# Performance work log

Hardware: AMD Instinct MI355X
Metric: run time of the kernel (lower is better)

The kernel has to match this reference:

```python
import jax, jax.numpy as jnp
import numpy as np

B, D, H, T, F = 2, 256, 8, 128, 64
C = H * F          # channels = 512
TE = 512           # time_embed_dim


def setup_inputs() -> dict:
    key = jax.random.key(0)
    ks = jax.random.split(key, 9)
    pd = jax.random.randint(ks[2], (B, T, T), 0, 2 * T - 1, dtype=jnp.int32) - (T - 1)
    s = 0.02
    return {
        "qk": jax.random.normal(ks[0], (B, D, H, T, F), jnp.float32),
        "temb": jax.random.normal(ks[1], (B, T, TE), jnp.float32),
        "pairwise_distances": pd,
        "w_dist": jax.random.normal(ks[3], (3, C), jnp.float32) * s,
        "b_dist": jax.random.normal(ks[4], (C,), jnp.float32) * s,
        "w_time": jax.random.normal(ks[5], (TE, C), jnp.float32) * s,
        "b_time": jax.random.normal(ks[6], (C,), jnp.float32) * s,
        "w_out": jax.random.normal(ks[7], (C, C), jnp.float32) * s,
        "b_out": jax.random.normal(ks[8], (C,), jnp.float32) * s,
    }


def _rpe_net(temb, pd, w_dist, b_dist, w_time, b_time, w_out, b_out):
    d = pd.astype(jnp.float32)
    # (B, T, S, 3): log(1+d+), log(1+d-), indicator(d==0)
    dist_embs = jnp.stack(
        [jnp.log1p(jnp.maximum(d, 0.0)),
         jnp.log1p(jnp.maximum(-d, 0.0)),
         (pd == 0).astype(jnp.float32)],
        axis=-1,
    )
    emb = (temb @ w_time + b_time)[:, :, None, :] + dist_embs @ w_dist + b_dist  # (B,T,S,C)
    R = jax.nn.silu(emb) @ w_out + b_out  # (B,T,S,C)
    return R.reshape(*pd.shape, H, F)     # (B,T,S,H,F)


def reference(qk, temb, pairwise_distances, w_dist, b_dist, w_time, b_time, w_out, b_out):
    R = _rpe_net(temb, pairwise_distances, w_dist, b_dist, w_time, b_time, w_out, b_out)
    # forward_qk: contract head_dim f for every (t, s) pair
    return jnp.einsum('bdhtf,btshf->bdhts', qk, R)
```

## Files before the change

### kernel.cpp

```cpp
#include <hip/hip_runtime.h>
#include <hip/hip_bf16.h>

#define B_  2
#define D_  256
#define H_  8
#define T_  128
#define S_  128
#define F_  64
#define C_  512
#define TE_ 512

typedef _Float16 f16x8 __attribute__((ext_vector_type(8)));
typedef _Float16 f16x4 __attribute__((ext_vector_type(4)));
typedef float    f32x4 __attribute__((ext_vector_type(4)));

__global__ __launch_bounds__(256) void k_time_proj(
    const float* __restrict__ temb, const float* __restrict__ w_time,
    const float* __restrict__ b_time, const float* __restrict__ b_dist,
    float* __restrict__ tp)
{
    int row0 = blockIdx.x * 2;
    int tid  = threadIdx.x;
    __shared__ float te[2][TE_];
    for (int i = tid; i < 2 * TE_; i += 256)
        te[i >> 9][i & 511] = temb[(size_t)row0 * TE_ + i];
    __syncthreads();
    for (int half = 0; half < 2; ++half) {
        int c = tid + half * 256;
        float bias = b_time[c] + b_dist[c];
        float a0 = bias, a1 = bias;
        for (int e = 0; e < TE_; ++e) {
            float w = w_time[(size_t)e * C_ + c];
            a0 += te[0][e] * w;
            a1 += te[1][e] * w;
        }
        tp[(size_t)row0 * C_ + c]       = a0;
        tp[(size_t)(row0 + 1) * C_ + c] = a1;
    }
}

__global__ __launch_bounds__(256) void k_wt(
    const float* __restrict__ w_out, _Float16* __restrict__ Wt)
{
    __shared__ float tile[64][65];
    int bn = blockIdx.x;
    int bk = blockIdx.y;
    int tx = threadIdx.x & 63;
    int ty = threadIdx.x >> 6;
#pragma unroll
    for (int p = 0; p < 16; ++p) {
        int row = p * 4 + ty;
        tile[row][tx] = w_out[(size_t)(bk * 64 + row) * C_ + bn * 64 + tx];
    }
    __syncthreads();
#pragma unroll
    for (int p = 0; p < 16; ++p) {
        int row = p * 4 + ty;
        Wt[(size_t)(bn * 64 + row) * C_ + bk * 64 + tx] = (_Float16)tile[tx][row];
    }
}

__global__ __launch_bounds__(256) void k_rpe_gemm(
    const float* __restrict__ tp, const int* __restrict__ pd,
    const float* __restrict__ w_dist, const _Float16* __restrict__ Wt,
    const float* __restrict__ b_out, _Float16* __restrict__ R)
{
    __shared__ _Float16 As[128][72];
    __shared__ _Float16 Bs[128][72];
    __shared__ float fs[3][128];
    __shared__ float tps[C_];
    __shared__ float wds[3][C_];
    int bm = blockIdx.x, bn = blockIdx.y;
    int tid = threadIdx.x;

    if (tid < 128) {
        int d = pd[bm * 128 + tid];
        fs[0][tid] = log1pf(fmaxf((float)d, 0.f));
        fs[1][tid] = log1pf(fmaxf((float)(-d), 0.f));
        fs[2][tid] = (d == 0) ? 1.f : 0.f;
    }
    for (int i = tid; i < C_; i += 256) tps[i] = tp[(size_t)bm * C_ + i];
    for (int i = tid; i < 3 * C_; i += 256) wds[i >> 9][i & 511] = w_dist[i];
    __syncthreads();

    int wave = tid >> 6, lane = tid & 63;
    int wm = (wave >> 1) * 64, wn = (wave & 1) * 64;
    int mrow = lane & 15, kq = (lane >> 4) * 8;
    int srow  = tid >> 1;
    int khalf = (tid & 1) * 32;
    int lrow = tid >> 3, lcol = (tid & 7) * 8;
    float f0 = fs[0][srow], f1 = fs[1][srow], f2 = fs[2][srow];

    f32x4 acc[4][4] = {};
    for (int k0 = 0; k0 < C_; k0 += 64) {
        _Float16 abuf[32];
#pragma unroll
        for (int kk = 0; kk < 32; ++kk) {
            int k = k0 + khalf + kk;
            float e = tps[k] + f0 * wds[0][k] + f1 * wds[1][k] + f2 * wds[2][k];
            e = e / (1.f + __expf(-e));
            abuf[kk] = (_Float16)e;
        }
#pragma unroll
        for (int v = 0; v < 4; ++v)
            *(f16x8*)&As[srow][khalf + v * 8] = *(const f16x8*)&abuf[v * 8];
#pragma unroll
        for (int p = 0; p < 4; ++p) {
            int r = p * 32 + lrow;
            *(f16x8*)&Bs[r][lcol] = *(const f16x8*)&Wt[(size_t)(bn * 128 + r) * C_ + k0 + lcol];
        }
        __syncthreads();
#pragma unroll
        for (int ks = 0; ks < 64; ks += 32) {
            f16x8 af[4], bfr[4];
#pragma unroll
            for (int i = 0; i < 4; ++i) af[i]  = *(const f16x8*)&As[wm + i * 16 + mrow][ks + kq];
#pragma unroll
            for (int j = 0; j < 4; ++j) bfr[j] = *(const f16x8*)&Bs[wn + j * 16 + mrow][ks + kq];
#pragma unroll
            for (int i = 0; i < 4; ++i)
#pragma unroll
                for (int j = 0; j < 4; ++j)
                    acc[i][j] = __builtin_amdgcn_mfma_f32_16x16x32_f16(af[i], bfr[j], acc[i][j], 0, 0, 0);
        }
        __syncthreads();
    }
    int col = lane & 15, rb = (lane >> 4) * 4;
    const size_t arow0 = (size_t)bm * 128;
#pragma unroll
    for (int j = 0; j < 4; ++j) {
        int n = bn * 128 + wn + j * 16 + col;
        float bo = b_out[n];
#pragma unroll
        for (int i = 0; i < 4; ++i)
#pragma unroll
            for (int r = 0; r < 4; ++r) {
                size_t m = arow0 + wm + i * 16 + rb + r;
                R[m * C_ + n] = (_Float16)(acc[i][j][r] + bo);
            }
    }
}

__global__ __launch_bounds__(256) void k_einsum(
    const float* __restrict__ qk, const _Float16* __restrict__ R,
    float* __restrict__ out)
{
    int bht  = blockIdx.x;
    int dblk = blockIdx.y;
    int t = bht & 127;
    int h = (bht >> 7) & 7;
    int b = bht >> 10;
    int tid = threadIdx.x;
    int wave = tid >> 6, lane = tid & 63;
    int wm = (wave >> 1) * 64, wn = (wave & 1) * 64;
    int mrow = lane & 15, kq = (lane >> 4) * 8;

    const size_t HTF = (size_t)H_ * T_ * F_;
    const float* qbase = qk + (size_t)b * D_ * HTF + (size_t)h * (T_ * F_)
                       + (size_t)t * F_ + (size_t)(dblk * 128) * HTF;
    const _Float16* rbase = R + ((size_t)(b * T_ + t) * S_) * C_ + h * 64;

    f32x4 acc[4][4] = {};
#pragma unroll
    for (int ks = 0; ks < 64; ks += 32) {
        f16x8 af[4], bfr[4];
#pragma unroll
        for (int i = 0; i < 4; ++i) {
            const float* p = qbase + (size_t)(wm + i * 16 + mrow) * HTF + ks + kq;
            float4 v0 = *(const float4*)p;
            float4 v1 = *(const float4*)(p + 4);
            f16x8 a;
            a[0] = (_Float16)v0.x; a[1] = (_Float16)v0.y;
            a[2] = (_Float16)v0.z; a[3] = (_Float16)v0.w;
            a[4] = (_Float16)v1.x; a[5] = (_Float16)v1.y;
            a[6] = (_Float16)v1.z; a[7] = (_Float16)v1.w;
            af[i] = a;
        }
#pragma unroll
        for (int j = 0; j < 4; ++j)
            bfr[j] = *(const f16x8*)(rbase + (size_t)(wn + j * 16 + mrow) * C_ + ks + kq);
#pragma unroll
        for (int i = 0; i < 4; ++i)
#pragma unroll
            for (int j = 0; j < 4; ++j)
                acc[i][j] = __builtin_amdgcn_mfma_f32_16x16x32_f16(af[i], bfr[j], acc[i][j], 0, 0, 0);
    }

    const size_t obase = (size_t)b * ((size_t)D_ * H_ * T_ * S_) + (size_t)h * (T_ * S_)
                       + (size_t)t * S_ + (size_t)(dblk * 128) * ((size_t)H_ * T_ * S_);
    int col = lane & 15, rb = (lane >> 4) * 4;
#pragma unroll
    for (int i = 0; i < 4; ++i)
#pragma unroll
        for (int r = 0; r < 4; ++r) {
            int dloc = wm + i * 16 + rb + r;
            size_t o = obase + (size_t)dloc * ((size_t)H_ * T_ * S_);
#pragma unroll
            for (int j = 0; j < 4; ++j)
                out[o + wn + j * 16 + col] = acc[i][j][r];
        }
}

extern "C" void kernel_launch(void* const* d_in, const int* in_sizes, int n_in,
                              void* d_out, int out_size, void* d_ws, size_t ws_size,
                              hipStream_t stream) {
    (void)in_sizes; (void)n_in; (void)out_size; (void)ws_size;
    const float* qk     = (const float*)d_in[0];
    const float* temb   = (const float*)d_in[1];
    const int*   pd     = (const int*)d_in[2];
    const float* w_dist = (const float*)d_in[3];
    const float* b_dist = (const float*)d_in[4];
    const float* w_time = (const float*)d_in[5];
    const float* b_time = (const float*)d_in[6];
    const float* w_out  = (const float*)d_in[7];
    const float* b_out  = (const float*)d_in[8];
    float* out = (float*)d_out;

    char* ws = (char*)d_ws;
    float*     tp = (float*)ws;
    _Float16*  Wt = (_Float16*)(ws + 512 * 1024);
    _Float16*  R  = (_Float16*)(ws + 1024 * 1024);

    k_time_proj<<<dim3(B_ * T_ / 2), dim3(256), 0, stream>>>(temb, w_time, b_time, b_dist, tp);
    k_wt<<<dim3(8, 8), dim3(256), 0, stream>>>(w_out, Wt);
    k_rpe_gemm<<<dim3(256, 4), dim3(256), 0, stream>>>(tp, pd, w_dist, Wt, b_out, R);
    k_einsum<<<dim3(B_ * H_ * T_, 2), dim3(256), 0, stream>>>(qk, R, out);
}
```

Baseline: 541.8 us.

## Split embed+SiLU out of RPE GEMM, widen time projection, use nontemporal einsum IO

The SiLU embedding is no longer recomputed inside each GEMM tile for every N-block. It is now produced once by a separate kernel into a half-precision A buffer in workspace, which the GEMM then loads. The time-projection kernel now handles four rows per block, so each w_time load is reused more. The einsum kernel uses nontemporal loads for qk and nontemporal stores for the output to avoid polluting the cache. In exchange, an extra 32 MB buffer round-trips through memory, and there is one more kernel launch.

```diff
diff --git a/kernel.cpp b/kernel.cpp
--- a/kernel.cpp
+++ b/kernel.cpp
@@ -19,23 +19,33 @@
     const float* __restrict__ b_time, const float* __restrict__ b_dist,
     float* __restrict__ tp)
 {
-    int row0 = blockIdx.x * 2;
+    int row0 = blockIdx.x * 4;
     int tid  = threadIdx.x;
-    __shared__ float te[2][TE_];
-    for (int i = tid; i < 2 * TE_; i += 256)
+    __shared__ float te[4][TE_];
+    for (int i = tid; i < 4 * TE_; i += 256)
         te[i >> 9][i & 511] = temb[(size_t)row0 * TE_ + i];
     __syncthreads();
-    for (int half = 0; half < 2; ++half) {
-        int c = tid + half * 256;
-        float bias = b_time[c] + b_dist[c];
-        float a0 = bias, a1 = bias;
-        for (int e = 0; e < TE_; ++e) {
-            float w = w_time[(size_t)e * C_ + c];
-            a0 += te[0][e] * w;
-            a1 += te[1][e] * w;
-        }
-        tp[(size_t)row0 * C_ + c]       = a0;
-        tp[(size_t)(row0 + 1) * C_ + c] = a1;
+    int c0 = tid, c1 = tid + 256;
+    float bias0 = b_time[c0] + b_dist[c0];
+    float bias1 = b_time[c1] + b_dist[c1];
+    float a[4][2];
+#pragma unroll
+    for (int r = 0; r < 4; ++r) { a[r][0] = bias0; a[r][1] = bias1; }
+#pragma unroll 4
+    for (int e = 0; e < TE_; ++e) {
+        float w0 = w_time[(size_t)e * C_ + c0];
+        float w1 = w_time[(size_t)e * C_ + c1];
+#pragma unroll
+        for (int r = 0; r < 4; ++r) {
+            float t = te[r][e];
+            a[r][0] += t * w0;
+            a[r][1] += t * w1;
+        }
+    }
+#pragma unroll
+    for (int r = 0; r < 4; ++r) {
+        tp[(size_t)(row0 + r) * C_ + c0] = a[r][0];
+        tp[(size_t)(row0 + r) * C_ + c1] = a[r][1];
     }
 }
 
@@ -60,54 +70,59 @@
     }
 }
 
-__global__ __launch_bounds__(256) void k_rpe_gemm(
+__global__ __launch_bounds__(256) void k_embed_silu(
     const float* __restrict__ tp, const int* __restrict__ pd,
-    const float* __restrict__ w_dist, const _Float16* __restrict__ Wt,
+    const float* __restrict__ w_dist, _Float16* __restrict__ A)
+{
+    int row = blockIdx.x * 8 + (threadIdx.x >> 5);
+    int bt  = row >> 7;
+    int d   = pd[row];
+    float f0 = log1pf(fmaxf((float)d, 0.f));
+    float f1 = log1pf(fmaxf((float)(-d), 0.f));
+    float f2 = (d == 0) ? 1.f : 0.f;
+    int c0 = (threadIdx.x & 31) * 16;
+    _Float16 buf[16];
+#pragma unroll
+    for (int v = 0; v < 4; ++v) {
+        int c = c0 + v * 4;
+        float4 t4 = *(const float4*)&tp[(size_t)bt * C_ + c];
+        float4 w0 = *(const float4*)&w_dist[c];
+        float4 w1 = *(const float4*)&w_dist[C_ + c];
+        float4 w2 = *(const float4*)&w_dist[2 * C_ + c];
+        float e0 = t4.x + f0 * w0.x + f1 * w1.x + f2 * w2.x;
+        float e1 = t4.y + f0 * w0.y + f1 * w1.y + f2 * w2.y;
+        float e2 = t4.z + f0 * w0.z + f1 * w1.z + f2 * w2.z;
+        float e3 = t4.w + f0 * w0.w + f1 * w1.w + f2 * w2.w;
+        buf[v * 4 + 0] = (_Float16)(e0 / (1.f + __expf(-e0)));
+        buf[v * 4 + 1] = (_Float16)(e1 / (1.f + __expf(-e1)));
+        buf[v * 4 + 2] = (_Float16)(e2 / (1.f + __expf(-e2)));
+        buf[v * 4 + 3] = (_Float16)(e3 / (1.f + __expf(-e3)));
+    }
+    *(f16x8*)&A[(size_t)row * C_ + c0]     = *(const f16x8*)&buf[0];
+    *(f16x8*)&A[(size_t)row * C_ + c0 + 8] = *(const f16x8*)&buf[8];
+}
+
+__global__ __launch_bounds__(256) void k_gemm_R(
+    const _Float16* __restrict__ A, const _Float16* __restrict__ Wt,
     const float* __restrict__ b_out, _Float16* __restrict__ R)
 {
+    const int K = 512, N = 512;
     __shared__ _Float16 As[128][72];
     __shared__ _Float16 Bs[128][72];
-    __shared__ float fs[3][128];
-    __shared__ float tps[C_];
-    __shared__ float wds[3][C_];
     int bm = blockIdx.x, bn = blockIdx.y;
     int tid = threadIdx.x;
-
-    if (tid < 128) {
-        int d = pd[bm * 128 + tid];
-        fs[0][tid] = log1pf(fmaxf((float)d, 0.f));
-        fs[1][tid] = log1pf(fmaxf((float)(-d), 0.f));
-        fs[2][tid] = (d == 0) ? 1.f : 0.f;
-    }
-    for (int i = tid; i < C_; i += 256) tps[i] = tp[(size_t)bm * C_ + i];
-    for (int i = tid; i < 3 * C_; i += 256) wds[i >> 9][i & 511] = w_dist[i];
-    __syncthreads();
-
     int wave = tid >> 6, lane = tid & 63;
     int wm = (wave >> 1) * 64, wn = (wave & 1) * 64;
     int mrow = lane & 15, kq = (lane >> 4) * 8;
-    int srow  = tid >> 1;
-    int khalf = (tid & 1) * 32;
     int lrow = tid >> 3, lcol = (tid & 7) * 8;
-    float f0 = fs[0][srow], f1 = fs[1][srow], f2 = fs[2][srow];
-
+    const size_t arow0 = (size_t)bm * 128;
     f32x4 acc[4][4] = {};
-    for (int k0 = 0; k0 < C_; k0 += 64) {
-        _Float16 abuf[32];
-#pragma unroll
-        for (int kk = 0; kk < 32; ++kk) {
-            int k = k0 + khalf + kk;
-            float e = tps[k] + f0 * wds[0][k] + f1 * wds[1][k] + f2 * wds[2][k];
-            e = e / (1.f + __expf(-e));
-            abuf[kk] = (_Float16)e;
-        }
-#pragma unroll
-        for (int v = 0; v < 4; ++v)
-            *(f16x8*)&As[srow][khalf + v * 8] = *(const f16x8*)&abuf[v * 8];
+    for (int k0 = 0; k0 < K; k0 += 64) {
 #pragma unroll
         for (int p = 0; p < 4; ++p) {
             int r = p * 32 + lrow;
-            *(f16x8*)&Bs[r][lcol] = *(const f16x8*)&Wt[(size_t)(bn * 128 + r) * C_ + k0 + lcol];
+            *(f16x8*)&As[r][lcol] = *(const f16x8*)&A[(arow0 + r) * K + k0 + lcol];
+            *(f16x8*)&Bs[r][lcol] = *(const f16x8*)&Wt[(size_t)(bn * 128 + r) * K + k0 + lcol];
         }
         __syncthreads();
 #pragma unroll
@@ -126,7 +141,6 @@
         __syncthreads();
     }
     int col = lane & 15, rb = (lane >> 4) * 4;
-    const size_t arow0 = (size_t)bm * 128;
 #pragma unroll
     for (int j = 0; j < 4; ++j) {
         int n = bn * 128 + wn + j * 16 + col;
@@ -136,7 +150,7 @@
 #pragma unroll
             for (int r = 0; r < 4; ++r) {
                 size_t m = arow0 + wm + i * 16 + rb + r;
-                R[m * C_ + n] = (_Float16)(acc[i][j][r] + bo);
+                R[m * N + n] = (_Float16)(acc[i][j][r] + bo);
             }
     }
 }
@@ -166,14 +180,14 @@
         f16x8 af[4], bfr[4];
 #pragma unroll
         for (int i = 0; i < 4; ++i) {
-            const float* p = qbase + (size_t)(wm + i * 16 + mrow) * HTF + ks + kq;
-            float4 v0 = *(const float4*)p;
-            float4 v1 = *(const float4*)(p + 4);
+            const f32x4* p = (const f32x4*)(qbase + (size_t)(wm + i * 16 + mrow) * HTF + ks + kq);
+            f32x4 v0 = __builtin_nontemporal_load(p);
+            f32x4 v1 = __builtin_nontemporal_load(p + 1);
             f16x8 a;
-            a[0] = (_Float16)v0.x; a[1] = (_Float16)v0.y;
-            a[2] = (_Float16)v0.z; a[3] = (_Float16)v0.w;
-            a[4] = (_Float16)v1.x; a[5] = (_Float16)v1.y;
-            a[6] = (_Float16)v1.z; a[7] = (_Float16)v1.w;
+            a[0] = (_Float16)v0[0]; a[1] = (_Float16)v0[1];
+            a[2] = (_Float16)v0[2]; a[3] = (_Float16)v0[3];
+            a[4] = (_Float16)v1[0]; a[5] = (_Float16)v1[1];
+            a[6] = (_Float16)v1[2]; a[7] = (_Float16)v1[3];
             af[i] = a;
         }
 #pragma unroll
@@ -197,7 +211,7 @@
             size_t o = obase + (size_t)dloc * ((size_t)H_ * T_ * S_);
 #pragma unroll
             for (int j = 0; j < 4; ++j)
-                out[o + wn + j * 16 + col] = acc[i][j][r];
+                __builtin_nontemporal_store(acc[i][j][r], &out[o + wn + j * 16 + col]);
         }
 }
 
@@ -219,10 +233,12 @@
     char* ws = (char*)d_ws;
     float*     tp = (float*)ws;
     _Float16*  Wt = (_Float16*)(ws + 512 * 1024);
-    _Float16*  R  = (_Float16*)(ws + 1024 * 1024);
-
-    k_time_proj<<<dim3(B_ * T_ / 2), dim3(256), 0, stream>>>(temb, w_time, b_time, b_dist, tp);
+    _Float16*  A  = (_Float16*)(ws + 1024 * 1024);
+    _Float16*  R  = (_Float16*)(ws + 1024 * 1024 + 33554432);
+
+    k_time_proj<<<dim3(B_ * T_ / 4), dim3(256), 0, stream>>>(temb, w_time, b_time, b_dist, tp);
     k_wt<<<dim3(8, 8), dim3(256), 0, stream>>>(w_out, Wt);
-    k_rpe_gemm<<<dim3(256, 4), dim3(256), 0, stream>>>(tp, pd, w_dist, Wt, b_out, R);
+    k_embed_silu<<<dim3(B_ * T_ * S_ / 8), dim3(256), 0, stream>>>(tp, pd, w_dist, A);
+    k_gemm_R<<<dim3(256, 4), dim3(256), 0, stream>>>(A, Wt, b_out, R);
     k_einsum<<<dim3(B_ * H_ * T_, 2), dim3(256), 0, stream>>>(qk, R, out);
 }
```

New measurement: 537.6 us. Within noise of the previous version (-0.8%).
